# Kernel optimization log

Hardware: AMD Instinct MI355X
Metric: run time of the kernel (lower is better)

## Reference

```python
import jax, jax.numpy as jnp
import numpy as np

EMBED_DIM = 1024
B, S = 8, 4096

def setup_inputs() -> dict:
    key = jax.random.key(0)
    k_x, k_w1, k_b1, k_phi, k_w2, k_b2 = jax.random.split(key, 6)
    lim1 = 1.0 / np.sqrt(EMBED_DIM)
    lim2 = 1.0  # linear2 fan_in = ffn_dim = 1
    return {
        "x": jax.random.normal(k_x, (B, S, EMBED_DIM), dtype=jnp.float32),
        "W1": jax.random.uniform(k_w1, (1, EMBED_DIM), jnp.float32, -lim1, lim1),
        "b1": jax.random.uniform(k_b1, (1,), jnp.float32, -lim1, lim1),
        "phi": jax.random.uniform(k_phi, (), jnp.float32, 0.0, 2.0 * np.pi),
        "W2": jax.random.uniform(k_w2, (EMBED_DIM, 1), jnp.float32, -lim2, lim2),
        "b2": jax.random.uniform(k_b2, (EMBED_DIM,), jnp.float32, -lim2, lim2),
    }

def reference(x, W1, b1, phi, W2, b2):
    # linear1: per-token projection to a scalar angle theta  [B,S,1]
    theta = jnp.einsum("bsd,od->bso", x, W1) + b1
    # 1-qubit circuit RY(theta) -> RX(phi) -> <PauliZ> on |0>
    # closed form: <Z> = cos(theta) * cos(phi)
    q = jnp.cos(theta) * jnp.cos(phi)  # [B,S,1]
    # dropout=0 (eval); linear2: ffn_dim(=1) -> embed_dim
    out = jnp.einsum("bso,do->bsd", q, W2) + b2  # [B,S,EMBED_DIM]
    return out
```

## Files before the change

### kernel.cpp

```cpp
#include <hip/hip_runtime.h>
#include <math.h>


#define EMBED_D 1024

__global__ __launch_bounds__(256) void ffq_kernel(
    const float* __restrict__ x,
    const float* __restrict__ W1,
    const float* __restrict__ b1,
    const float* __restrict__ phi,
    const float* __restrict__ W2,
    const float* __restrict__ b2,
    float* __restrict__ out)
{
    const int tok = blockIdx.x;
    const int t   = threadIdx.x;

    const float4* x4  = (const float4*)(x + (size_t)tok * EMBED_D);
    const float4* w14 = (const float4*)W1;
    float4 xv = x4[t];
    float4 wv = w14[t];
    float v = xv.x * wv.x + xv.y * wv.y + xv.z * wv.z + xv.w * wv.w;

    #pragma unroll
    for (int off = 32; off > 0; off >>= 1)
        v += __shfl_down(v, off, 64);

    __shared__ float partial[4];
    __shared__ float qsh;
    if ((t & 63) == 0) partial[t >> 6] = v;
    __syncthreads();

    if (t == 0) {
        float theta = partial[0] + partial[1] + partial[2] + partial[3] + b1[0];
        qsh = cosf(theta) * cosf(phi[0]);
    }
    __syncthreads();
    const float q = qsh;

    const float4* w24 = (const float4*)W2;
    const float4* b24 = (const float4*)b2;
    float4 w2v = w24[t];
    float4 b2v = b24[t];
    float4 o;
    o.x = fmaf(q, w2v.x, b2v.x);
    o.y = fmaf(q, w2v.y, b2v.y);
    o.z = fmaf(q, w2v.z, b2v.z);
    o.w = fmaf(q, w2v.w, b2v.w);
    ((float4*)(out + (size_t)tok * EMBED_D))[t] = o;
}

extern "C" void kernel_launch(void* const* d_in, const int* in_sizes, int n_in,
                              void* d_out, int out_size, void* d_ws, size_t ws_size,
                              hipStream_t stream) {
    const float* x   = (const float*)d_in[0];
    const float* W1  = (const float*)d_in[1];
    const float* b1  = (const float*)d_in[2];
    const float* phi = (const float*)d_in[3];
    const float* W2  = (const float*)d_in[4];
    const float* b2  = (const float*)d_in[5];
    float* out = (float*)d_out;

    const int ntok = in_sizes[0] / EMBED_D;
    ffq_kernel<<<ntok, 256, 0, stream>>>(x, W1, b1, phi, W2, b2, out);
}
```

Measured before the change: 229.3 us.

## Process one token per wavefront with persistent grid-stride loop and nontemporal IO

Each 64-lane wavefront now handles a whole token, reducing the dot product with xor shuffles and no shared memory or block barriers. A fixed grid of 2048 blocks loops over tokens, so the W1, W2 and b2 vectors are loaded into registers once per wave instead of once per token. Loads of x and stores of out use nontemporal hints to avoid polluting the cache. This costs more registers per thread and fixes the grid size independent of the problem.

```diff
diff --git a/kernel.cpp b/kernel.cpp
--- a/kernel.cpp
+++ b/kernel.cpp
@@ -3,6 +3,8 @@
 
 
 #define EMBED_D 1024
+
+typedef float floatx4 __attribute__((ext_vector_type(4)));
 
 __global__ __launch_bounds__(256) void ffq_kernel(
     const float* __restrict__ x,
@@ -11,43 +13,61 @@
     const float* __restrict__ phi,
     const float* __restrict__ W2,
     const float* __restrict__ b2,
-    float* __restrict__ out)
+    float* __restrict__ out,
+    int ntok)
 {
-    const int tok = blockIdx.x;
-    const int t   = threadIdx.x;
+    const int lane   = threadIdx.x & 63;
+    const int wave   = (int)((blockIdx.x * blockDim.x + threadIdx.x) >> 6);
+    const int nwaves = (int)((gridDim.x * blockDim.x) >> 6);
 
-    const float4* x4  = (const float4*)(x + (size_t)tok * EMBED_D);
-    const float4* w14 = (const float4*)W1;
-    float4 xv = x4[t];
-    float4 wv = w14[t];
-    float v = xv.x * wv.x + xv.y * wv.y + xv.z * wv.z + xv.w * wv.w;
+    const float cphi = cosf(phi[0]);
+    const float bias = b1[0];
 
+    const floatx4* w14 = (const floatx4*)W1;
+    const floatx4* w24 = (const floatx4*)W2;
+    const floatx4* b24 = (const floatx4*)b2;
+
+    floatx4 w1v[4], w2v[4], b2v[4];
     #pragma unroll
-    for (int off = 32; off > 0; off >>= 1)
-        v += __shfl_down(v, off, 64);
+    for (int j = 0; j < 4; ++j) {
+        w1v[j] = w14[lane + 64 * j];
+        w2v[j] = w24[lane + 64 * j];
+        b2v[j] = b24[lane + 64 * j];
+    }
 
-    __shared__ float partial[4];
-    __shared__ float qsh;
-    if ((t & 63) == 0) partial[t >> 6] = v;
-    __syncthreads();
+    for (int tok = wave; tok < ntok; tok += nwaves) {
+        const floatx4* x4 = (const floatx4*)(x + (size_t)tok * EMBED_D);
+        floatx4 xv[4];
+        #pragma unroll
+        for (int j = 0; j < 4; ++j)
+            xv[j] = __builtin_nontemporal_load(&x4[lane + 64 * j]);
 
-    if (t == 0) {
-        float theta = partial[0] + partial[1] + partial[2] + partial[3] + b1[0];
-        qsh = cosf(theta) * cosf(phi[0]);
+        float v = 0.f;
+        #pragma unroll
+        for (int j = 0; j < 4; ++j) {
+            v = fmaf(xv[j].x, w1v[j].x, v);
+            v = fmaf(xv[j].y, w1v[j].y, v);
+            v = fmaf(xv[j].z, w1v[j].z, v);
+            v = fmaf(xv[j].w, w1v[j].w, v);
+        }
+
+        #pragma unroll
+        for (int off = 1; off < 64; off <<= 1)
+            v += __shfl_xor(v, off, 64);
+
+        const float q = cosf(v + bias) * cphi;
+
+        floatx4* o4 = (floatx4*)(out + (size_t)tok * EMBED_D);
+        #pragma unroll
+        for (int j = 0; j < 4; ++j) {
+            floatx4 o;
+            o.x = fmaf(q, w2v[j].x, b2v[j].x);
+            o.y = fmaf(q, w2v[j].y, b2v[j].y);
+            o.z = fmaf(q, w2v[j].z, b2v[j].z);
+            o.w = fmaf(q, w2v[j].w, b2v[j].w);
+            __builtin_nontemporal_store(o, &o4[lane + 64 * j]);
+        }
     }
-    __syncthreads();
-    const float q = qsh;
-
-    const float4* w24 = (const float4*)W2;
-    const float4* b24 = (const float4*)b2;
-    float4 w2v = w24[t];
-    float4 b2v = b24[t];
-    float4 o;
-    o.x = fmaf(q, w2v.x, b2v.x);
-    o.y = fmaf(q, w2v.y, b2v.y);
-    o.z = fmaf(q, w2v.z, b2v.z);
-    o.w = fmaf(q, w2v.w, b2v.w);
-    ((float4*)(out + (size_t)tok * EMBED_D))[t] = o;
 }
 
 extern "C" void kernel_launch(void* const* d_in, const int* in_sizes, int n_in,
@@ -62,5 +82,5 @@
     float* out = (float*)d_out;
 
     const int ntok = in_sizes[0] / EMBED_D;
-    ffq_kernel<<<ntok, 256, 0, stream>>>(x, W1, b1, phi, W2, b2, out);
+    ffq_kernel<<<2048, 256, 0, stream>>>(x, W1, b1, phi, W2, b2, out, ntok);
 }
```

New measurement: 230.2 us. Within noise of the previous version (+0.4%).
